# Kernel tuning notes

Measured on AMD Instinct MI355X. Metric: run time of the kernel, lower is better.

## Reference

```python
import jax, jax.numpy as jnp
import numpy as np

N, E, B = 50000, 800000, 64     # nodes, edges, graphs
IN, H = 3, 64                   # in_channels, hidden_channels
NDEF = 6
EPS = 1e-5                      # BatchNorm eps


def setup_inputs() -> dict:
    key = jax.random.key(0)
    ks = jax.random.split(key, 32)

    def lin(k, fi, fo):
        kw, kb = jax.random.split(k)
        s = 1.0 / np.sqrt(fi)
        W = jax.random.uniform(kw, (fi, fo), jnp.float32, -s, s)
        b = jax.random.uniform(kb, (fo,), jnp.float32, -s, s)
        return W, b

    inp = {}
    inp["x"] = jax.random.normal(ks[0], (N, IN), jnp.float32)
    inp["edge_index"] = jax.random.randint(ks[1], (2, E), 0, N, jnp.int64)
    inp["batch"] = jnp.sort(jax.random.randint(ks[2], (N,), 0, B, jnp.int64))

    inp["W1"], inp["b1"] = lin(ks[3], IN, H)
    inp["W2"], inp["b2"] = lin(ks[4], H, H)
    inp["W3"], inp["b3"] = lin(ks[5], H, H)
    for i, kk in zip((1, 2, 3), (ks[6], ks[7], ks[8])):
        kg, kb2 = jax.random.split(kk)
        inp[f"bn{i}_g"] = 1.0 + 0.1 * jax.random.normal(kg, (H,), jnp.float32)
        inp[f"bn{i}_b"] = 0.1 * jax.random.normal(kb2, (H,), jnp.float32)
        inp[f"bn{i}_m"] = jnp.zeros((H,), jnp.float32)
        inp[f"bn{i}_v"] = jnp.ones((H,), jnp.float32)

    inp["th_W1"], inp["th_b1"] = lin(ks[9], H, H // 2)
    inp["th_W2"], inp["th_b2"] = lin(ks[10], H // 2, NDEF)
    inp["lh_W1"], inp["lh_b1"] = lin(ks[11], H, H // 2)
    inp["lh_W2"], inp["lh_b2"] = lin(ks[12], H // 2, 2)
    inp["sh_W1"], inp["sh_b1"] = lin(ks[13], H, H // 4)
    inp["sh_W2"], inp["sh_b2"] = lin(ks[14], H // 4, 1)
    return inp


def reference(x, edge_index, batch,
              W1, b1, W2, b2, W3, b3,
              bn1_g, bn1_b, bn1_m, bn1_v,
              bn2_g, bn2_b, bn2_m, bn2_v,
              bn3_g, bn3_b, bn3_m, bn3_v,
              th_W1, th_b1, th_W2, th_b2,
              lh_W1, lh_b1, lh_W2, lh_b2,
              sh_W1, sh_b1, sh_W2, sh_b2):
    src, dst = edge_index[0], edge_index[1]
    # GCN symmetric normalization with self-loops: deg counts in-edges + self
    deg = jax.ops.segment_sum(jnp.ones((E,), x.dtype), dst, num_segments=N) + 1.0
    dis = jax.lax.rsqrt(deg)                 # deg^{-1/2}  [N]
    enorm = (dis[src] * dis[dst])[:, None]   # per-edge norm
    snorm = (dis * dis)[:, None]             # self-loop norm

    def gcn(h, W, b):
        m = h @ W  # [N, H]
        agg = jax.ops.segment_sum(m[src] * enorm, dst, num_segments=N) + m * snorm
        return agg + b

    def bn(h, g, beta, mu, var):
        return (h - mu) * jax.lax.rsqrt(var + EPS) * g + beta

    h = jax.nn.relu(bn(gcn(x, W1, b1), bn1_g, bn1_b, bn1_m, bn1_v))
    h = jax.nn.relu(bn(gcn(h, W2, b2), bn2_g, bn2_b, bn2_m, bn2_v))
    h = jax.nn.relu(bn(gcn(h, W3, b3), bn3_g, bn3_b, bn3_m, bn3_v))

    # global_mean_pool over graphs
    cnt = jax.ops.segment_sum(jnp.ones((N,), h.dtype), batch, num_segments=B)
    gemb = jax.ops.segment_sum(h, batch, num_segments=B) / jnp.maximum(cnt, 1.0)[:, None]

    type_logits = jax.nn.relu(gemb @ th_W1 + th_b1) @ th_W2 + th_b2
    location = jax.nn.sigmoid(jax.nn.relu(gemb @ lh_W1 + lh_b1) @ lh_W2 + lh_b2)
    severity = jax.nn.sigmoid(jax.nn.relu(gemb @ sh_W1 + sh_b1) @ sh_W2 + sh_b2)
    return (type_logits, location, severity)
```

## Files before the change

### kernel.cpp

```cpp
#include <hip/hip_runtime.h>
#include <hip/hip_bf16.h>
#include <math.h>

#define HH 64
#define EPS 1e-5f
#define STAGE_CAP 12288
#define NBLK_SCAT 192
#define PER_LANE 3

__device__ __forceinline__ int lower_bound_i(const int* a, int n, int key) {
    int lo = 0, hi = n;
    while (lo < hi) { int mid = (lo + hi) >> 1; if (a[mid] < key) lo = mid + 1; else hi = mid; }
    return lo;
}

__device__ __forceinline__ unsigned short f2bf(float f) {
    unsigned int u = __float_as_uint(f);
    unsigned int r = (u + 0x7FFFu + ((u >> 16) & 1u)) >> 16;
    return (unsigned short)r;
}
__device__ __forceinline__ float bf2f(unsigned short b) {
    return __uint_as_float(((unsigned int)b) << 16);
}
__device__ __forceinline__ float bflo(unsigned int u) { return __uint_as_float(u << 16); }
__device__ __forceinline__ float bfhi(unsigned int u) { return __uint_as_float(u & 0xFFFF0000u); }

__global__ void init_kernel(float* gsum, int NG) {
    int t = blockIdx.x * blockDim.x + threadIdx.x;
    if (t < NG) gsum[t] = 0.f;
}

__global__ __launch_bounds__(256) void hist_kernel(const int* __restrict__ dst,
        int* __restrict__ blockhist, int E, int chunk) {
    __shared__ int hist[256];
    int tid = threadIdx.x, blk = blockIdx.x;
    hist[tid] = 0;
    __syncthreads();
    int s = blk * chunk, e = s + chunk; if (e > E) e = E;
    for (int i = s + tid; i < e; i += 256) atomicAdd(&hist[dst[i] >> 8], 1);
    __syncthreads();
    blockhist[blk * 256 + tid] = hist[tid];
}

__global__ __launch_bounds__(256) void bucketscan_kernel(const int* __restrict__ blockhist,
        int* __restrict__ bucketbase, int NB, int E) {
    __shared__ int wsum2[4];
    int tid = threadIdx.x, lane = tid & 63, wid = tid >> 6;
    int s = 0;
    if (tid < NB) {
        for (int i = 0; i < NBLK_SCAT; ++i) s += blockhist[i * 256 + tid];
    }
    int incl = s;
    #pragma unroll
    for (int off = 1; off < 64; off <<= 1) {
        int n = __shfl_up(incl, off);
        if (lane >= off) incl += n;
    }
    if (lane == 63) wsum2[wid] = incl;
    __syncthreads();
    int wbase = 0;
    #pragma unroll
    for (int k = 0; k < 4; ++k) if (k < wid) wbase += wsum2[k];
    if (tid < NB) bucketbase[tid] = wbase + incl - s;
    if (tid == 0) bucketbase[NB] = E;
}

__global__ __launch_bounds__(64) void offsets_kernel(const int* __restrict__ bucketbase,
        int* __restrict__ blockhist, int NB) {
    int b = blockIdx.x;
    int lane = threadIdx.x;
    int v[PER_LANE];
    int base = lane * PER_LANE;
    int s = 0;
    #pragma unroll
    for (int k = 0; k < PER_LANE; ++k) {
        int i = base + k;
        v[k] = (i < NBLK_SCAT) ? blockhist[i * 256 + b] : 0;
        s += v[k];
    }
    int incl = s;
    #pragma unroll
    for (int off = 1; off < 64; off <<= 1) {
        int n = __shfl_up(incl, off);
        if (lane >= off) incl += n;
    }
    int excl = incl - s + bucketbase[b];
    #pragma unroll
    for (int k = 0; k < PER_LANE; ++k) {
        int i = base + k;
        if (i < NBLK_SCAT) { blockhist[i * 256 + b] = excl; excl += v[k]; }
    }
}

__global__ __launch_bounds__(256) void scatterA_kernel(const int* __restrict__ src,
        const int* __restrict__ dst, const int* __restrict__ blockhist,
        int* __restrict__ buf, int E, int chunk) {
    __shared__ int lcur[256];
    int tid = threadIdx.x, blk = blockIdx.x;
    lcur[tid] = blockhist[blk * 256 + tid];
    __syncthreads();
    int s = blk * chunk, e = s + chunk; if (e > E) e = E;
    for (int i = s + tid; i < e; i += 256) {
        int d = dst[i];
        int b = d >> 8;
        int p = atomicAdd(&lcur[b], 1);
        buf[p] = ((d & 255) << 24) | src[i];
    }
}

__global__ __launch_bounds__(256) void bucket_to_csr_kernel(const int* __restrict__ buf,
        const int* __restrict__ bucketbase, int* __restrict__ rowstart,
        float* __restrict__ dis, int* __restrict__ csr, int N, int E) {
    __shared__ int ldeg[256];
    __shared__ int cur[256];
    __shared__ int wsum2[4];
    __shared__ int stage[STAGE_CAP];
    int b = blockIdx.x;
    int nodeStart = b << 8;
    int nodeEnd = nodeStart + 256; if (nodeEnd > N) nodeEnd = N;
    int nloc = nodeEnd - nodeStart;
    int base = bucketbase[b];
    int nE = bucketbase[b + 1] - base;
    int tid = threadIdx.x;
    int lane = tid & 63, wid = tid >> 6;
    ldeg[tid] = 0;
    __syncthreads();
    for (int i = tid; i < nE; i += 256)
        atomicAdd(&ldeg[((unsigned)buf[base + i]) >> 24], 1);
    __syncthreads();
    int d = ldeg[tid];
    int incl = d;
    #pragma unroll
    for (int off = 1; off < 64; off <<= 1) {
        int n = __shfl_up(incl, off);
        if (lane >= off) incl += n;
    }
    if (lane == 63) wsum2[wid] = incl;
    __syncthreads();
    int wbase = 0;
    #pragma unroll
    for (int k = 0; k < 4; ++k) if (k < wid) wbase += wsum2[k];
    int excl = wbase + incl - d;
    cur[tid] = excl;
    if (tid < nloc) {
        rowstart[nodeStart + tid] = base + excl;
        dis[nodeStart + tid] = rsqrtf((float)d + 1.0f);
    }
    if (b == 0 && tid == 0) rowstart[N] = E;
    __syncthreads();
    if (nE <= STAGE_CAP) {
        for (int i = tid; i < nE; i += 256) {
            int u = buf[base + i];
            int l = ((unsigned)u) >> 24;
            int p = atomicAdd(&cur[l], 1);
            stage[p] = u & 0xFFFFFF;
        }
        __syncthreads();
        for (int i = tid; i < nE; i += 256) csr[base + i] = stage[i];
    } else {
        for (int i = tid; i < nE; i += 256) {
            int u = buf[base + i];
            int l = ((unsigned)u) >> 24;
            int p = atomicAdd(&cur[l], 1);
            csr[base + p] = u & 0xFFFFFF;
        }
    }
}

__global__ void mt1_kernel(const float* __restrict__ x, const float* __restrict__ W1,
                           const float* __restrict__ dis, unsigned int* __restrict__ mt2, int N) {
    int t = blockIdx.x * blockDim.x + threadIdx.x;
    if (t < N * 32) {
        int v = t >> 5, c2 = t & 31;
        float x0 = x[v * 3 + 0], x1 = x[v * 3 + 1], x2 = x[v * 3 + 2];
        float dv = dis[v];
        float ma = (x0 * W1[0 * HH + 2 * c2] + x1 * W1[1 * HH + 2 * c2] + x2 * W1[2 * HH + 2 * c2]) * dv;
        float mb = (x0 * W1[0 * HH + 2 * c2 + 1] + x1 * W1[1 * HH + 2 * c2 + 1] + x2 * W1[2 * HH + 2 * c2 + 1]) * dv;
        mt2[t] = (unsigned)f2bf(ma) | ((unsigned)f2bf(mb) << 16);
    }
}

__global__ __launch_bounds__(256) void gemm_scale_kernel(const float* __restrict__ h,
        const float* __restrict__ W, const float* __restrict__ dis,
        unsigned short* __restrict__ mt, int N) {
    __shared__ unsigned int wsp[HH * 34];
    __shared__ unsigned int hs2[64 * 34];
    int tid = threadIdx.x;
    int lane = tid & 63, wid = tid >> 6;
    {
        int c = tid & 63;
        for (int k2 = tid >> 6; k2 < 32; k2 += 4) {
            float a = W[(2 * k2) * HH + c];
            float b = W[(2 * k2 + 1) * HH + c];
            wsp[c * 34 + k2] = (unsigned)f2bf(a) | ((unsigned)f2bf(b) << 16);
        }
    }
    int v0 = blockIdx.x * 64;
    int nv = N - v0; if (nv > 64) nv = 64;
    for (int idx = tid; idx < 64 * 32; idx += 256) {
        int n = idx >> 5, k2 = idx & 31;
        int vsrc = v0 + ((n < nv) ? n : 0);
        float a = h[(size_t)vsrc * HH + 2 * k2];
        float b = h[(size_t)vsrc * HH + 2 * k2 + 1];
        hs2[n * 34 + k2] = (unsigned)f2bf(a) | ((unsigned)f2bf(b) << 16);
    }
    __syncthreads();
    for (int n = wid * 16; n < wid * 16 + 16; ++n) {
        int vg = v0 + n;
        if (n >= nv) break;
        float acc = 0.f;
        #pragma unroll 4
        for (int k2g = 0; k2g < 16; ++k2g) {
            uint2 wv = *(const uint2*)&wsp[lane * 34 + 2 * k2g];
            uint2 hv = *(const uint2*)&hs2[n * 34 + 2 * k2g];
            acc = fmaf(bflo(hv.x), bflo(wv.x), acc);
            acc = fmaf(bfhi(hv.x), bfhi(wv.x), acc);
            acc = fmaf(bflo(hv.y), bflo(wv.y), acc);
            acc = fmaf(bfhi(hv.y), bfhi(wv.y), acc);
        }
        mt[(size_t)vg * HH + lane] = f2bf(acc * dis[vg]);
    }
}

__global__ __launch_bounds__(256) void gather_bn_kernel(const unsigned short* __restrict__ mt,
        const int* __restrict__ rowstart, const int* __restrict__ csr_src,
        const float* __restrict__ dis, const float* __restrict__ bias,
        const float* __restrict__ gam, const float* __restrict__ beta,
        const float* __restrict__ mu, const float* __restrict__ var,
        float* __restrict__ hout, int N) {
    int lane = threadIdx.x & 63, wid = threadIdx.x >> 6;
    int v = blockIdx.x * 4 + wid;
    if (v >= N) return;
    int half = lane >> 5;
    int hl = lane & 31;
    int start = rowstart[v], end = rowstart[v + 1];
    float ax = 0.f, ay = 0.f;
    if (half == 0) {
        unsigned u = *(const unsigned*)&mt[(size_t)v * HH + 2 * hl];
        ax = bflo(u); ay = bfhi(u);
    }
    for (int base = start; base < end; base += 64) {
        int idx = (base + lane < end) ? csr_src[base + lane] : 0;
        int cnt = end - base; if (cnt > 64) cnt = 64;
        int j = 0;
        for (; j + 15 < cnt; j += 16) {
            int p0 = __shfl(idx, j + 0 + half);
            int p1 = __shfl(idx, j + 2 + half);
            int p2 = __shfl(idx, j + 4 + half);
            int p3 = __shfl(idx, j + 6 + half);
            int p4 = __shfl(idx, j + 8 + half);
            int p5 = __shfl(idx, j + 10 + half);
            int p6 = __shfl(idx, j + 12 + half);
            int p7 = __shfl(idx, j + 14 + half);
            unsigned u0 = *(const unsigned*)&mt[(size_t)p0 * HH + 2 * hl];
            unsigned u1 = *(const unsigned*)&mt[(size_t)p1 * HH + 2 * hl];
            unsigned u2 = *(const unsigned*)&mt[(size_t)p2 * HH + 2 * hl];
            unsigned u3 = *(const unsigned*)&mt[(size_t)p3 * HH + 2 * hl];
            unsigned u4 = *(const unsigned*)&mt[(size_t)p4 * HH + 2 * hl];
            unsigned u5 = *(const unsigned*)&mt[(size_t)p5 * HH + 2 * hl];
            unsigned u6 = *(const unsigned*)&mt[(size_t)p6 * HH + 2 * hl];
            unsigned u7 = *(const unsigned*)&mt[(size_t)p7 * HH + 2 * hl];
            ax += bflo(u0); ay += bfhi(u0);
            ax += bflo(u1); ay += bfhi(u1);
            ax += bflo(u2); ay += bfhi(u2);
            ax += bflo(u3); ay += bfhi(u3);
            ax += bflo(u4); ay += bfhi(u4);
            ax += bflo(u5); ay += bfhi(u5);
            ax += bflo(u6); ay += bfhi(u6);
            ax += bflo(u7); ay += bfhi(u7);
        }
        for (; j + 1 < cnt; j += 2) {
            int p = __shfl(idx, j + half);
            unsigned u = *(const unsigned*)&mt[(size_t)p * HH + 2 * hl];
            ax += bflo(u); ay += bfhi(u);
        }
        if (j < cnt) {
            int p = __shfl(idx, j);
            if (half == 0) {
                unsigned u = *(const unsigned*)&mt[(size_t)p * HH + 2 * hl];
                ax += bflo(u); ay += bfhi(u);
            }
        }
    }
    float ox = __shfl_xor(ax, 32);
    float oy = __shfl_xor(ay, 32);
    if (half == 0) {
        ax += ox; ay += oy;
        float dv = dis[v];
        float2 bi = *(const float2*)&bias[2 * hl];
        float2 gm = *(const float2*)&gam[2 * hl];
        float2 be = *(const float2*)&beta[2 * hl];
        float2 mm = *(const float2*)&mu[2 * hl];
        float2 vv = *(const float2*)&var[2 * hl];
        float vx = (ax * dv + bi.x - mm.x) * rsqrtf(vv.x + EPS) * gm.x + be.x;
        float vy = (ay * dv + bi.y - mm.y) * rsqrtf(vv.y + EPS) * gm.y + be.y;
        float2 o = make_float2(fmaxf(vx, 0.f), fmaxf(vy, 0.f));
        *(float2*)&hout[(size_t)v * HH + 2 * hl] = o;
    }
}

__global__ __launch_bounds__(256) void pool_partial_kernel(const float* __restrict__ h,
        const int* __restrict__ batch, float* __restrict__ gsum, int N, int chunk) {
    int lane = threadIdx.x & 63, wid = threadIdx.x >> 6;
    int w = blockIdx.x * 4 + wid;
    int start = w * chunk;
    int end = start + chunk; if (end > N) end = N;
    if (start >= end) return;
    int g = batch[start];
    float acc = 0.f;
    for (int i = start; i < end; ++i) {
        int gi = batch[i];
        if (gi != g) {
            atomicAdd(&gsum[g * HH + lane], acc);
            acc = 0.f; g = gi;
        }
        acc += h[i * HH + lane];
    }
    atomicAdd(&gsum[g * HH + lane], acc);
}

__global__ __launch_bounds__(64) void heads_kernel(const float* __restrict__ gsum,
        const int* __restrict__ batch, int N,
        const float* __restrict__ thW1, const float* __restrict__ thb1,
        const float* __restrict__ thW2, const float* __restrict__ thb2,
        const float* __restrict__ lhW1, const float* __restrict__ lhb1,
        const float* __restrict__ lhW2, const float* __restrict__ lhb2,
        const float* __restrict__ shW1, const float* __restrict__ shb1,
        const float* __restrict__ shW2, const float* __restrict__ shb2,
        float* __restrict__ out, int B) {
    int g = blockIdx.x, t = threadIdx.x;
    __shared__ float ge[HH];
    __shared__ float hT[32], hL[32], hS[16];
    int lo = lower_bound_i(batch, N, g);
    int hi = lower_bound_i(batch, N, g + 1);
    float cnt = (float)(hi - lo);
    ge[t] = gsum[g * HH + t] / fmaxf(cnt, 1.0f);
    __syncthreads();
    if (t < 32) {
        float a = thb1[t];
        for (int k = 0; k < HH; ++k) a += ge[k] * thW1[k * 32 + t];
        hT[t] = fmaxf(a, 0.f);
    } else {
        int j = t - 32;
        float a = lhb1[j];
        for (int k = 0; k < HH; ++k) a += ge[k] * lhW1[k * 32 + j];
        hL[j] = fmaxf(a, 0.f);
    }
    __syncthreads();
    if (t < 16) {
        float a = shb1[t];
        for (int k = 0; k < HH; ++k) a += ge[k] * shW1[k * 16 + t];
        hS[t] = fmaxf(a, 0.f);
    }
    __syncthreads();
    if (t < 6) {
        float a = thb2[t];
        for (int j = 0; j < 32; ++j) a += hT[j] * thW2[j * 6 + t];
        out[g * 6 + t] = a;
    } else if (t >= 8 && t < 10) {
        int o = t - 8;
        float a = lhb2[o];
        for (int j = 0; j < 32; ++j) a += hL[j] * lhW2[j * 2 + o];
        out[B * 6 + g * 2 + o] = 1.f / (1.f + expf(-a));
    } else if (t == 12) {
        float a = shb2[0];
        for (int j = 0; j < 16; ++j) a += hS[j] * shW2[j];
        out[B * 8 + g] = 1.f / (1.f + expf(-a));
    }
}

extern "C" void kernel_launch(void* const* d_in, const int* in_sizes, int n_in,
                              void* d_out, int out_size, void* d_ws, size_t ws_size,
                              hipStream_t stream) {
    const float* x   = (const float*)d_in[0];
    const int*   ei  = (const int*)d_in[1];
    const int*   bat = (const int*)d_in[2];
    const float* W1 = (const float*)d_in[3];  const float* b1 = (const float*)d_in[4];
    const float* W2 = (const float*)d_in[5];  const float* b2 = (const float*)d_in[6];
    const float* W3 = (const float*)d_in[7];  const float* b3 = (const float*)d_in[8];
    const float* bn1g = (const float*)d_in[9];  const float* bn1b = (const float*)d_in[10];
    const float* bn1m = (const float*)d_in[11]; const float* bn1v = (const float*)d_in[12];
    const float* bn2g = (const float*)d_in[13]; const float* bn2b = (const float*)d_in[14];
    const float* bn2m = (const float*)d_in[15]; const float* bn2v = (const float*)d_in[16];
    const float* bn3g = (const float*)d_in[17]; const float* bn3b = (const float*)d_in[18];
    const float* bn3m = (const float*)d_in[19]; const float* bn3v = (const float*)d_in[20];
    const float* thW1 = (const float*)d_in[21]; const float* thb1 = (const float*)d_in[22];
    const float* thW2 = (const float*)d_in[23]; const float* thb2 = (const float*)d_in[24];
    const float* lhW1 = (const float*)d_in[25]; const float* lhb1 = (const float*)d_in[26];
    const float* lhW2 = (const float*)d_in[27]; const float* lhb2 = (const float*)d_in[28];
    const float* shW1 = (const float*)d_in[29]; const float* shb1 = (const float*)d_in[30];
    const float* shW2 = (const float*)d_in[31]; const float* shb2 = (const float*)d_in[32];
    float* out = (float*)d_out;

    const int N = in_sizes[0] / 3;
    const int E = in_sizes[1] / 2;
    const int B = out_size / 9;
    const int NB = (N + 255) >> 8;
    const int* esrc = ei;
    const int* edst = ei + E;

    char* w = (char*)d_ws;
    size_t off = 0;
    auto alloc = [&](size_t bytes) -> void* {
        void* p = w + off;
        off += (bytes + 255) & ~(size_t)255;
        return p;
    };
    int*   rowstart   = (int*)  alloc((size_t)(N + 1) * 4);
    float* dis        = (float*)alloc((size_t)N * 4);
    int*   csr        = (int*)  alloc((size_t)E * 4);
    int*   blockhist  = (int*)  alloc((size_t)NBLK_SCAT * 256 * 4);
    int*   bucketbase = (int*)  alloc((size_t)(NB + 1) * 4);
    float* hbuf       = (float*)alloc((size_t)N * HH * 4);
    unsigned short* mtbuf = (unsigned short*)alloc((size_t)N * HH * 2);
    float* gsum       = (float*)alloc((size_t)B * HH * 4);
    int*   bucketbuf  = (int*)mtbuf;
    (void)ws_size;

    const int TB = 256;
    const int echunk = (E + NBLK_SCAT - 1) / NBLK_SCAT;
    init_kernel<<<(B * HH + TB - 1) / TB, TB, 0, stream>>>(gsum, B * HH);
    hist_kernel<<<NBLK_SCAT, TB, 0, stream>>>(edst, blockhist, E, echunk);
    bucketscan_kernel<<<1, TB, 0, stream>>>(blockhist, bucketbase, NB, E);
    offsets_kernel<<<NB, 64, 0, stream>>>(bucketbase, blockhist, NB);
    scatterA_kernel<<<NBLK_SCAT, TB, 0, stream>>>(esrc, edst, blockhist, bucketbuf, E, echunk);
    bucket_to_csr_kernel<<<NB, TB, 0, stream>>>(bucketbuf, bucketbase, rowstart, dis, csr, N, E);

    int gatherBlocks = (N + 3) / 4;
    int gemmBlocks = (N + 63) / 64;
    mt1_kernel<<<(N * 32 + TB - 1) / TB, TB, 0, stream>>>(x, W1, dis, (unsigned int*)mtbuf, N);
    gather_bn_kernel<<<gatherBlocks, TB, 0, stream>>>(mtbuf, rowstart, csr, dis,
            b1, bn1g, bn1b, bn1m, bn1v, hbuf, N);
    gemm_scale_kernel<<<gemmBlocks, TB, 0, stream>>>(hbuf, W2, dis, mtbuf, N);
    gather_bn_kernel<<<gatherBlocks, TB, 0, stream>>>(mtbuf, rowstart, csr, dis,
            b2, bn2g, bn2b, bn2m, bn2v, hbuf, N);
    gemm_scale_kernel<<<gemmBlocks, TB, 0, stream>>>(hbuf, W3, dis, mtbuf, N);
    gather_bn_kernel<<<gatherBlocks, TB, 0, stream>>>(mtbuf, rowstart, csr, dis,
            b3, bn3g, bn3b, bn3m, bn3v, hbuf, N);

    const int PW_BLOCKS = 512;
    int chunk = (N + PW_BLOCKS * 4 - 1) / (PW_BLOCKS * 4);
    pool_partial_kernel<<<PW_BLOCKS, TB, 0, stream>>>(hbuf, bat, gsum, N, chunk);

    heads_kernel<<<B, 64, 0, stream>>>(gsum, bat, N, thW1, thb1, thW2, thb2,
            lhW1, lhb1, lhW2, lhb2, shW1, shb1, shW2, shb2, out, B);
}
```

Baseline: 218.1 us.

## Split message table into two channel halves and gather each half separately

Result: slower. 262.3 us (+20.3%).

```diff
diff --git a/kernel.cpp b/kernel.cpp
--- a/kernel.cpp
+++ b/kernel.cpp
@@ -168,21 +168,25 @@
 }
 
 __global__ void mt1_kernel(const float* __restrict__ x, const float* __restrict__ W1,
-                           const float* __restrict__ dis, unsigned int* __restrict__ mt2, int N) {
+                           const float* __restrict__ dis,
+                           unsigned int* __restrict__ mtL2, unsigned int* __restrict__ mtH2, int N) {
     int t = blockIdx.x * blockDim.x + threadIdx.x;
     if (t < N * 32) {
         int v = t >> 5, c2 = t & 31;
         float x0 = x[v * 3 + 0], x1 = x[v * 3 + 1], x2 = x[v * 3 + 2];
         float dv = dis[v];
-        float ma = (x0 * W1[0 * HH + 2 * c2] + x1 * W1[1 * HH + 2 * c2] + x2 * W1[2 * HH + 2 * c2]) * dv;
-        float mb = (x0 * W1[0 * HH + 2 * c2 + 1] + x1 * W1[1 * HH + 2 * c2 + 1] + x2 * W1[2 * HH + 2 * c2 + 1]) * dv;
-        mt2[t] = (unsigned)f2bf(ma) | ((unsigned)f2bf(mb) << 16);
+        int c = 2 * c2;
+        float ma = (x0 * W1[0 * HH + c] + x1 * W1[1 * HH + c] + x2 * W1[2 * HH + c]) * dv;
+        float mb = (x0 * W1[0 * HH + c + 1] + x1 * W1[1 * HH + c + 1] + x2 * W1[2 * HH + c + 1]) * dv;
+        unsigned pk = (unsigned)f2bf(ma) | ((unsigned)f2bf(mb) << 16);
+        if (c2 < 16) mtL2[v * 16 + c2] = pk;
+        else         mtH2[v * 16 + (c2 - 16)] = pk;
     }
 }
 
 __global__ __launch_bounds__(256) void gemm_scale_kernel(const float* __restrict__ h,
         const float* __restrict__ W, const float* __restrict__ dis,
-        unsigned short* __restrict__ mt, int N) {
+        unsigned short* __restrict__ mtL, unsigned short* __restrict__ mtH, int N) {
     __shared__ unsigned int wsp[HH * 34];
     __shared__ unsigned int hs2[64 * 34];
     int tid = threadIdx.x;
@@ -205,6 +209,8 @@
         hs2[n * 34 + k2] = (unsigned)f2bf(a) | ((unsigned)f2bf(b) << 16);
     }
     __syncthreads();
+    unsigned short* tbl = (lane < 32) ? mtL : mtH;
+    int cl = lane & 31;
     for (int n = wid * 16; n < wid * 16 + 16; ++n) {
         int vg = v0 + n;
         if (n >= nv) break;
@@ -218,25 +224,24 @@
             acc = fmaf(bflo(hv.y), bflo(wv.y), acc);
             acc = fmaf(bfhi(hv.y), bfhi(wv.y), acc);
         }
-        mt[(size_t)vg * HH + lane] = f2bf(acc * dis[vg]);
-    }
-}
-
-__global__ __launch_bounds__(256) void gather_bn_kernel(const unsigned short* __restrict__ mt,
+        tbl[(size_t)vg * 32 + cl] = f2bf(acc * dis[vg]);
+    }
+}
+
+__global__ __launch_bounds__(256) void gather_bn_half_kernel(const unsigned short* __restrict__ mth,
         const int* __restrict__ rowstart, const int* __restrict__ csr_src,
         const float* __restrict__ dis, const float* __restrict__ bias,
         const float* __restrict__ gam, const float* __restrict__ beta,
         const float* __restrict__ mu, const float* __restrict__ var,
-        float* __restrict__ hout, int N) {
+        float* __restrict__ hout, int N, int co) {
     int lane = threadIdx.x & 63, wid = threadIdx.x >> 6;
     int v = blockIdx.x * 4 + wid;
     if (v >= N) return;
-    int half = lane >> 5;
-    int hl = lane & 31;
+    int r = lane >> 4, c4 = lane & 15;
     int start = rowstart[v], end = rowstart[v + 1];
     float ax = 0.f, ay = 0.f;
-    if (half == 0) {
-        unsigned u = *(const unsigned*)&mt[(size_t)v * HH + 2 * hl];
+    if (r == 0) {
+        unsigned u = *(const unsigned*)&mth[(size_t)v * 32 + 2 * c4];
         ax = bflo(u); ay = bfhi(u);
     }
     for (int base = start; base < end; base += 64) {
@@ -244,58 +249,40 @@
         int cnt = end - base; if (cnt > 64) cnt = 64;
         int j = 0;
         for (; j + 15 < cnt; j += 16) {
-            int p0 = __shfl(idx, j + 0 + half);
-            int p1 = __shfl(idx, j + 2 + half);
-            int p2 = __shfl(idx, j + 4 + half);
-            int p3 = __shfl(idx, j + 6 + half);
-            int p4 = __shfl(idx, j + 8 + half);
-            int p5 = __shfl(idx, j + 10 + half);
-            int p6 = __shfl(idx, j + 12 + half);
-            int p7 = __shfl(idx, j + 14 + half);
-            unsigned u0 = *(const unsigned*)&mt[(size_t)p0 * HH + 2 * hl];
-            unsigned u1 = *(const unsigned*)&mt[(size_t)p1 * HH + 2 * hl];
-            unsigned u2 = *(const unsigned*)&mt[(size_t)p2 * HH + 2 * hl];
-            unsigned u3 = *(const unsigned*)&mt[(size_t)p3 * HH + 2 * hl];
-            unsigned u4 = *(const unsigned*)&mt[(size_t)p4 * HH + 2 * hl];
-            unsigned u5 = *(const unsigned*)&mt[(size_t)p5 * HH + 2 * hl];
-            unsigned u6 = *(const unsigned*)&mt[(size_t)p6 * HH + 2 * hl];
-            unsigned u7 = *(const unsigned*)&mt[(size_t)p7 * HH + 2 * hl];
+            int p0 = __shfl(idx, j + r);
+            int p1 = __shfl(idx, j + 4 + r);
+            int p2 = __shfl(idx, j + 8 + r);
+            int p3 = __shfl(idx, j + 12 + r);
+            unsigned u0 = *(const unsigned*)&mth[(size_t)p0 * 32 + 2 * c4];
+            unsigned u1 = *(const unsigned*)&mth[(size_t)p1 * 32 + 2 * c4];
+            unsigned u2 = *(const unsigned*)&mth[(size_t)p2 * 32 + 2 * c4];
+            unsigned u3 = *(const unsigned*)&mth[(size_t)p3 * 32 + 2 * c4];
             ax += bflo(u0); ay += bfhi(u0);
             ax += bflo(u1); ay += bfhi(u1);
             ax += bflo(u2); ay += bfhi(u2);
             ax += bflo(u3); ay += bfhi(u3);
-            ax += bflo(u4); ay += bfhi(u4);
-            ax += bflo(u5); ay += bfhi(u5);
-            ax += bflo(u6); ay += bfhi(u6);
-            ax += bflo(u7); ay += bfhi(u7);
-        }
-        for (; j + 1 < cnt; j += 2) {
-            int p = __shfl(idx, j + half);
-            unsigned u = *(const unsigned*)&mt[(size_t)p * HH + 2 * hl];
+        }
+        for (; j + 3 < cnt; j += 4) {
+            int p = __shfl(idx, j + r);
+            unsigned u = *(const unsigned*)&mth[(size_t)p * 32 + 2 * c4];
             ax += bflo(u); ay += bfhi(u);
         }
         if (j < cnt) {
-            int p = __shfl(idx, j);
-            if (half == 0) {
-                unsigned u = *(const unsigned*)&mt[(size_t)p * HH + 2 * hl];
-                ax += bflo(u); ay += bfhi(u);
-            }
-        }
-    }
-    float ox = __shfl_xor(ax, 32);
-    float oy = __shfl_xor(ay, 32);
-    if (half == 0) {
-        ax += ox; ay += oy;
+            int jr = j + r;
+            int p = __shfl(idx, (jr < cnt) ? jr : 0);
+            float m = (jr < cnt) ? 1.f : 0.f;
+            unsigned u = *(const unsigned*)&mth[(size_t)p * 32 + 2 * c4];
+            ax += m * bflo(u); ay += m * bfhi(u);
+        }
+    }
+    ax += __shfl_xor(ax, 16); ay += __shfl_xor(ay, 16);
+    ax += __shfl_xor(ax, 32); ay += __shfl_xor(ay, 32);
+    if (r == 0) {
+        int c = co + 2 * c4;
         float dv = dis[v];
-        float2 bi = *(const float2*)&bias[2 * hl];
-        float2 gm = *(const float2*)&gam[2 * hl];
-        float2 be = *(const float2*)&beta[2 * hl];
-        float2 mm = *(const float2*)&mu[2 * hl];
-        float2 vv = *(const float2*)&var[2 * hl];
-        float vx = (ax * dv + bi.x - mm.x) * rsqrtf(vv.x + EPS) * gm.x + be.x;
-        float vy = (ay * dv + bi.y - mm.y) * rsqrtf(vv.y + EPS) * gm.y + be.y;
-        float2 o = make_float2(fmaxf(vx, 0.f), fmaxf(vy, 0.f));
-        *(float2*)&hout[(size_t)v * HH + 2 * hl] = o;
+        float vx = (ax * dv + bias[c]     - mu[c])     * rsqrtf(var[c] + EPS)     * gam[c]     + beta[c];
+        float vy = (ay * dv + bias[c + 1] - mu[c + 1]) * rsqrtf(var[c + 1] + EPS) * gam[c + 1] + beta[c + 1];
+        *(float2*)&hout[(size_t)v * HH + c] = make_float2(fmaxf(vx, 0.f), fmaxf(vy, 0.f));
     }
 }
 
@@ -412,9 +399,10 @@
     int*   blockhist  = (int*)  alloc((size_t)NBLK_SCAT * 256 * 4);
     int*   bucketbase = (int*)  alloc((size_t)(NB + 1) * 4);
     float* hbuf       = (float*)alloc((size_t)N * HH * 4);
-    unsigned short* mtbuf = (unsigned short*)alloc((size_t)N * HH * 2);
+    unsigned short* mtL = (unsigned short*)alloc((size_t)N * 32 * 2);
+    unsigned short* mtH = (unsigned short*)alloc((size_t)N * 32 * 2);
     float* gsum       = (float*)alloc((size_t)B * HH * 4);
-    int*   bucketbuf  = (int*)mtbuf;
+    int*   bucketbuf  = (int*)hbuf;
     (void)ws_size;
 
     const int TB = 256;
@@ -428,15 +416,22 @@
 
     int gatherBlocks = (N + 3) / 4;
     int gemmBlocks = (N + 63) / 64;
-    mt1_kernel<<<(N * 32 + TB - 1) / TB, TB, 0, stream>>>(x, W1, dis, (unsigned int*)mtbuf, N);
-    gather_bn_kernel<<<gatherBlocks, TB, 0, stream>>>(mtbuf, rowstart, csr, dis,
-            b1, bn1g, bn1b, bn1m, bn1v, hbuf, N);
-    gemm_scale_kernel<<<gemmBlocks, TB, 0, stream>>>(hbuf, W2, dis, mtbuf, N);
-    gather_bn_kernel<<<gatherBlocks, TB, 0, stream>>>(mtbuf, rowstart, csr, dis,
-            b2, bn2g, bn2b, bn2m, bn2v, hbuf, N);
-    gemm_scale_kernel<<<gemmBlocks, TB, 0, stream>>>(hbuf, W3, dis, mtbuf, N);
-    gather_bn_kernel<<<gatherBlocks, TB, 0, stream>>>(mtbuf, rowstart, csr, dis,
-            b3, bn3g, bn3b, bn3m, bn3v, hbuf, N);
+    mt1_kernel<<<(N * 32 + TB - 1) / TB, TB, 0, stream>>>(x, W1, dis,
+            (unsigned int*)mtL, (unsigned int*)mtH, N);
+    gather_bn_half_kernel<<<gatherBlocks, TB, 0, stream>>>(mtL, rowstart, csr, dis,
+            b1, bn1g, bn1b, bn1m, bn1v, hbuf, N, 0);
+    gather_bn_half_kernel<<<gatherBlocks, TB, 0, stream>>>(mtH, rowstart, csr, dis,
+            b1, bn1g, bn1b, bn1m, bn1v, hbuf, N, 32);
+    gemm_scale_kernel<<<gemmBlocks, TB, 0, stream>>>(hbuf, W2, dis, mtL, mtH, N);
+    gather_bn_half_kernel<<<gatherBlocks, TB, 0, stream>>>(mtL, rowstart, csr, dis,
+            b2, bn2g, bn2b, bn2m, bn2v, hbuf, N, 0);
+    gather_bn_half_kernel<<<gatherBlocks, TB, 0, stream>>>(mtH, rowstart, csr, dis,
+            b2, bn2g, bn2b, bn2m, bn2v, hbuf, N, 32);
+    gemm_scale_kernel<<<gemmBlocks, TB, 0, stream>>>(hbuf, W3, dis, mtL, mtH, N);
+    gather_bn_half_kernel<<<gatherBlocks, TB, 0, stream>>>(mtL, rowstart, csr, dis,
+            b3, bn3g, bn3b, bn3m, bn3v, hbuf, N, 0);
+    gather_bn_half_kernel<<<gatherBlocks, TB, 0, stream>>>(mtH, rowstart, csr, dis,
+            b3, bn3g, bn3b, bn3m, bn3v, hbuf, N, 32);
 
     const int PW_BLOCKS = 512;
     int chunk = (N + PW_BLOCKS * 4 - 1) / (PW_BLOCKS * 4);
```
